# Performance work log

Hardware: AMD Instinct MI355X
Metric: run time of the kernel (lower is better)

Reference implementation:

```python
import jax, jax.numpy as jnp
import numpy as np

H = 64  # hidden_size

def _gru_layer(x_seq, Wih, Whh, bih, bhh):
    """PyTorch-semantics GRU layer. x_seq: [B, T, D] -> [B, T, H].
    Gate order in weights is (r, z, n), matching nn.GRU."""
    B = x_seq.shape[0]
    # Precompute input projections for all timesteps at once: [B, T, 3H]
    x_proj = jnp.einsum('btd,gd->btg', x_seq, Wih) + bih
    x_proj = jnp.swapaxes(x_proj, 0, 1)  # [T, B, 3H] for scan

    def step(h, xp):
        hp = h @ Whh.T + bhh                      # [B, 3H]
        xr, xz, xn = jnp.split(xp, 3, axis=-1)
        hr, hz, hn = jnp.split(hp, 3, axis=-1)
        r = jax.nn.sigmoid(xr + hr)
        z = jax.nn.sigmoid(xz + hz)
        n = jnp.tanh(xn + r * hn)
        h_new = (1.0 - z) * n + z * h
        return h_new, h_new

    h0 = jnp.zeros((B, H), dtype=x_seq.dtype)
    _, hs = jax.lax.scan(step, h0, x_proj)        # hs: [T, B, H]
    return jnp.swapaxes(hs, 0, 1)                 # [B, T, H]


def setup_inputs() -> dict:
    key = jax.random.key(0)
    ks = jax.random.split(key, 12)
    B, T, D, O = 2048, 512, 1, 1
    s = 1.0 / np.sqrt(H)  # PyTorch GRU init scale
    return {
        'x':     jax.random.normal(ks[0], (B, T, D), jnp.float32),
        'W_ih0': jax.random.normal(ks[1], (3 * H, D), jnp.float32) * s,
        'W_hh0': jax.random.normal(ks[2], (3 * H, H), jnp.float32) * s,
        'b_ih0': jax.random.normal(ks[3], (3 * H,), jnp.float32) * s,
        'b_hh0': jax.random.normal(ks[4], (3 * H,), jnp.float32) * s,
        'W_ih1': jax.random.normal(ks[5], (3 * H, H), jnp.float32) * s,
        'W_hh1': jax.random.normal(ks[6], (3 * H, H), jnp.float32) * s,
        'b_ih1': jax.random.normal(ks[7], (3 * H,), jnp.float32) * s,
        'b_hh1': jax.random.normal(ks[8], (3 * H,), jnp.float32) * s,
        'W_fc':  jax.random.normal(ks[9], (O, H), jnp.float32) * s,
        'b_fc':  jax.random.normal(ks[10], (O,), jnp.float32) * s,
    }


def reference(x, W_ih0, W_hh0, b_ih0, b_hh0, W_ih1, W_hh1, b_ih1, b_hh1, W_fc, b_fc):
    h1 = _gru_layer(x, W_ih0, W_hh0, b_ih0, b_hh0)   # [B, T, H]
    h2 = _gru_layer(h1, W_ih1, W_hh1, b_ih1, b_hh1)  # [B, T, H]
    last = h2[:, -1, :]                              # [B, H]
    return last @ W_fc.T + b_fc                      # [B, O]
```

## Files before the change

### kernel.cpp

```cpp
#include <hip/hip_runtime.h>


#define T_LEN 512
#define BROWS 16
#define XPAD  513
#define LOG2E 1.44269504088896f

typedef float          f32x4 __attribute__((ext_vector_type(4)));
typedef __bf16         bf16x8 __attribute__((ext_vector_type(8)));
typedef unsigned short us8   __attribute__((ext_vector_type(8)));
typedef unsigned int   ui4   __attribute__((ext_vector_type(4)));
typedef unsigned int   ui2   __attribute__((ext_vector_type(2)));
typedef unsigned short ushort_t;

__device__ __forceinline__ float bf2f(ushort_t b){
    unsigned int u = ((unsigned int)b) << 16;
    return __uint_as_float(u);
}
__device__ __forceinline__ ushort_t f2bf(float f){
    unsigned int u = __float_as_uint(f);
    u = (u + 0x7FFFu + ((u >> 16) & 1u)) >> 16;
    return (ushort_t)u;
}
__device__ __forceinline__ float ld_any(const void* p, int i, bool f32){
    return f32 ? ((const float*)p)[i] : bf2f(((const ushort_t*)p)[i]);
}
__device__ __forceinline__ float exp2_fast(float x){
#if __has_builtin(__builtin_amdgcn_exp2f)
    return __builtin_amdgcn_exp2f(x);
#else
    return __expf(0.6931471805599453f * x);
#endif
}
__device__ __forceinline__ float rcp_fast(float x){
#if __has_builtin(__builtin_amdgcn_rcpf)
    return __builtin_amdgcn_rcpf(x);
#else
    return __fdividef(1.0f, x);
#endif
}
__device__ __forceinline__ float sigm2(float t){
    return rcp_fast(1.0f + exp2_fast(-t));
}
__device__ __forceinline__ float tanh2(float t){
    return fmaf(-2.0f, rcp_fast(exp2_fast(t) + 1.0f), 1.0f);
}
__device__ __forceinline__ f32x4 mfma16(bf16x8 a, bf16x8 b, f32x4 c){
    return __builtin_amdgcn_mfma_f32_16x16x32_bf16(a, b, c, 0, 0, 0);
}
__device__ __forceinline__ unsigned int cvtpk(float lo, float hi){
    unsigned int r;
    asm("v_cvt_pk_bf16_f32 %0, %1, %2" : "=v"(r) : "v"(lo), "v"(hi));
    return r;
}
__device__ __forceinline__ bf16x8 mk_frag(const void* W, int n, int kb, bool f32, float sc){
    us8 tmp;
    #pragma unroll
    for (int j = 0; j < 8; ++j){
        float v = f32 ? ((const float*)W)[n * 64 + kb + j]
                      : bf2f(((const ushort_t*)W)[n * 64 + kb + j]);
        tmp[j] = f2bf(v * sc);
    }
    return __builtin_bit_cast(bf16x8, tmp);
}

__global__ __launch_bounds__(512, 2) void gru_fused(
    const void* __restrict__ xv,
    const void* __restrict__ Wih0, const void* __restrict__ Whh0,
    const void* __restrict__ bih0, const void* __restrict__ bhh0,
    const void* __restrict__ Wih1, const void* __restrict__ Whh1,
    const void* __restrict__ bih1, const void* __restrict__ bhh1,
    const void* __restrict__ Wfc,  const void* __restrict__ bfc,
    void* __restrict__ outv)
{
    __shared__ float xbuf[BROWS * XPAD];
    __shared__ ui2   hAq[2][4][64];
    __shared__ ui2   hBq[2][4][64];
    __shared__ float fcb[4][16];

    const int tid   = threadIdx.x;
    const int wv    = tid >> 6;
    const int layer = wv >> 2;
    const int tau   = wv & 3;
    const int l  = tid & 63;
    const int b  = l & 15;
    const int hp = l >> 4;
    const int am = l & 15;
    const long row0 = (long)blockIdx.x * BROWS;

    bool f32 = false;
    {
        const ushort_t* xs = (const ushort_t*)xv;
        for (int j = 0; j < 64; ++j){
            int e = (xs[2 * j] >> 7) & 0xFF;
            if (e > 150) f32 = true;
        }
    }

    {
        ui2 z = {0u, 0u};
        ui2* pa = &hAq[0][0][0];
        ui2* pb = &hBq[0][0][0];
        for (int k = tid; k < 2 * 4 * 64; k += 512){ pa[k] = z; pb[k] = z; }
    }
    if (f32){
        for (int idx = tid; idx < BROWS * (T_LEN / 4); idx += 512){
            const int r = idx >> 7, sg = idx & 127;
            f32x4 v = ((const f32x4*)((const float*)xv + (row0 + r) * T_LEN))[sg];
            #pragma unroll
            for (int j = 0; j < 4; ++j) xbuf[r * XPAD + sg * 4 + j] = v[j];
        }
    } else {
        for (int idx = tid; idx < BROWS * (T_LEN / 8); idx += 512){
            const int r = idx >> 6, sg = idx & 63;
            us8 v = ((const us8*)((const ushort_t*)xv + (row0 + r) * T_LEN))[sg];
            #pragma unroll
            for (int j = 0; j < 8; ++j) xbuf[r * XPAD + sg * 8 + j] = bf2f(v[j]);
        }
    }

    const float gsc0 = LOG2E, gsc2 = 2.0f * LOG2E;

    bf16x8 wA[3][2];
    bf16x8 wH[3][2];
    f32x4 cbR, cbZ, cbNx, cbNh;
    f32x4 cwR, cwZ, cwN;
    const void* Wihp = layer ? Wih1 : Wih0;
    const void* Whhp = layer ? Whh1 : Whh0;
    const void* bihp = layer ? bih1 : bih0;
    const void* bhhp = layer ? bhh1 : bhh0;
    const int hb0 = 32 * (tau >> 1) + 8 * hp + 4 * (tau & 1);
    #pragma unroll
    for (int g = 0; g < 3; ++g){
        const float sc = (g == 2) ? gsc2 : gsc0;
        const int grow = g * 64 + 32 * (tau >> 1) + 8 * (am >> 2) + 4 * (tau & 1) + (am & 3);
        if (layer == 0){
            wA[g][0] = mk_frag(Whhp, grow, 8 * hp,      f32, sc);
            wA[g][1] = mk_frag(Whhp, grow, 32 + 8 * hp, f32, sc);
        } else {
            wA[g][0] = mk_frag(Wihp, grow, 8 * hp,      f32, sc);
            wA[g][1] = mk_frag(Wihp, grow, 32 + 8 * hp, f32, sc);
            wH[g][0] = mk_frag(Whhp, grow, 8 * hp,      f32, sc);
            wH[g][1] = mk_frag(Whhp, grow, 32 + 8 * hp, f32, sc);
        }
    }
    #pragma unroll
    for (int r = 0; r < 4; ++r){
        const int hc = hb0 + r;
        cbR[r]  = (ld_any(bihp, hc, f32)      + ld_any(bhhp, hc, f32))      * gsc0;
        cbZ[r]  = (ld_any(bihp, 64 + hc, f32) + ld_any(bhhp, 64 + hc, f32)) * gsc0;
        cbNx[r] = ld_any(bihp, 128 + hc, f32) * gsc2;
        cbNh[r] = ld_any(bhhp, 128 + hc, f32) * gsc2;
        if (layer == 0){
            cwR[r] = ld_any(Wih0, hc, f32)       * gsc0;
            cwZ[r] = ld_any(Wih0, 64 + hc, f32)  * gsc0;
            cwN[r] = ld_any(Wih0, 128 + hc, f32) * gsc2;
        }
    }

    f32x4 hS = {0.f, 0.f, 0.f, 0.f};

    __syncthreads();

    for (int t = 0; t < T_LEN; ++t){
        if (layer == 0){
            const int p = t & 1, pr = p ^ 1;
            ui2 q0 = hAq[pr][0][l], q1 = hAq[pr][1][l];
            ui2 q2 = hAq[pr][2][l], q3 = hAq[pr][3][l];
            ui4 u0 = {q0[0], q0[1], q1[0], q1[1]};
            ui4 u1 = {q2[0], q2[1], q3[0], q3[1]};
            bf16x8 B0 = __builtin_bit_cast(bf16x8, u0);
            bf16x8 B1 = __builtin_bit_cast(bf16x8, u1);
            const float xb = xbuf[b * XPAD + t];
            f32x4 aR, aZ, aX, aN;
            #pragma unroll
            for (int r = 0; r < 4; ++r){
                aR[r] = fmaf(xb, cwR[r], cbR[r]);
                aZ[r] = fmaf(xb, cwZ[r], cbZ[r]);
                aX[r] = fmaf(xb, cwN[r], cbNx[r]);
            }
            aR = mfma16(wA[0][0], B0, aR); aR = mfma16(wA[0][1], B1, aR);
            aZ = mfma16(wA[1][0], B0, aZ); aZ = mfma16(wA[1][1], B1, aZ);
            aN = mfma16(wA[2][0], B0, cbNh); aN = mfma16(wA[2][1], B1, aN);
            #pragma unroll
            for (int r = 0; r < 4; ++r){
                float rg = sigm2(aR[r]);
                float zg = sigm2(aZ[r]);
                float ng = tanh2(aX[r] + rg * aN[r]);
                hS[r] = ng + zg * (hS[r] - ng);
            }
            ui2 own = { cvtpk(hS[0], hS[1]), cvtpk(hS[2], hS[3]) };
            hAq[p][tau][l] = own;
        } else if (t > 0){
            const int pa = (t - 1) & 1, pb = pa ^ 1;
            ui2 a0 = hAq[pa][0][l], a1 = hAq[pa][1][l];
            ui2 a2 = hAq[pa][2][l], a3 = hAq[pa][3][l];
            ui2 c0 = hBq[pb][0][l], c1 = hBq[pb][1][l];
            ui2 c2 = hBq[pb][2][l], c3 = hBq[pb][3][l];
            ui4 ua0 = {a0[0], a0[1], a1[0], a1[1]};
            ui4 ua1 = {a2[0], a2[1], a3[0], a3[1]};
            ui4 ub0 = {c0[0], c0[1], c1[0], c1[1]};
            ui4 ub1 = {c2[0], c2[1], c3[0], c3[1]};
            bf16x8 gA0 = __builtin_bit_cast(bf16x8, ua0);
            bf16x8 gA1 = __builtin_bit_cast(bf16x8, ua1);
            bf16x8 B0  = __builtin_bit_cast(bf16x8, ub0);
            bf16x8 B1  = __builtin_bit_cast(bf16x8, ub1);
            f32x4 aR, aZ, aX, aN;
            aR = mfma16(wA[0][0], gA0, cbR);  aR = mfma16(wA[0][1], gA1, aR);
            aR = mfma16(wH[0][0], B0,  aR);   aR = mfma16(wH[0][1], B1,  aR);
            aZ = mfma16(wA[1][0], gA0, cbZ);  aZ = mfma16(wA[1][1], gA1, aZ);
            aZ = mfma16(wH[1][0], B0,  aZ);   aZ = mfma16(wH[1][1], B1,  aZ);
            aX = mfma16(wA[2][0], gA0, cbNx); aX = mfma16(wA[2][1], gA1, aX);
            aN = mfma16(wH[2][0], B0,  cbNh); aN = mfma16(wH[2][1], B1,  aN);
            #pragma unroll
            for (int r = 0; r < 4; ++r){
                float rg = sigm2(aR[r]);
                float zg = sigm2(aZ[r]);
                float ng = tanh2(aX[r] + rg * aN[r]);
                hS[r] = ng + zg * (hS[r] - ng);
            }
            ui2 own = { cvtpk(hS[0], hS[1]), cvtpk(hS[2], hS[3]) };
            hBq[pa][tau][l] = own;
        }
        __syncthreads();
    }

    if (layer == 1){
        ui2 a0 = hAq[1][0][l], a1 = hAq[1][1][l];
        ui2 a2 = hAq[1][2][l], a3 = hAq[1][3][l];
        ui2 c0 = hBq[0][0][l], c1 = hBq[0][1][l];
        ui2 c2 = hBq[0][2][l], c3 = hBq[0][3][l];
        ui4 ua0 = {a0[0], a0[1], a1[0], a1[1]};
        ui4 ua1 = {a2[0], a2[1], a3[0], a3[1]};
        ui4 ub0 = {c0[0], c0[1], c1[0], c1[1]};
        ui4 ub1 = {c2[0], c2[1], c3[0], c3[1]};
        bf16x8 gA0 = __builtin_bit_cast(bf16x8, ua0);
        bf16x8 gA1 = __builtin_bit_cast(bf16x8, ua1);
        bf16x8 B0  = __builtin_bit_cast(bf16x8, ub0);
        bf16x8 B1  = __builtin_bit_cast(bf16x8, ub1);
        f32x4 aR, aZ, aX, aN;
        aR = mfma16(wA[0][0], gA0, cbR);  aR = mfma16(wA[0][1], gA1, aR);
        aR = mfma16(wH[0][0], B0,  aR);   aR = mfma16(wH[0][1], B1,  aR);
        aZ = mfma16(wA[1][0], gA0, cbZ);  aZ = mfma16(wA[1][1], gA1, aZ);
        aZ = mfma16(wH[1][0], B0,  aZ);   aZ = mfma16(wH[1][1], B1,  aZ);
        aX = mfma16(wA[2][0], gA0, cbNx); aX = mfma16(wA[2][1], gA1, aX);
        aN = mfma16(wH[2][0], B0,  cbNh); aN = mfma16(wH[2][1], B1,  aN);
        float part = 0.0f;
        #pragma unroll
        for (int r = 0; r < 4; ++r){
            float rg = sigm2(aR[r]);
            float zg = sigm2(aZ[r]);
            float ng = tanh2(aX[r] + rg * aN[r]);
            float hf = ng + zg * (hS[r] - ng);
            part = fmaf(ld_any(Wfc, hb0 + r, f32), hf, part);
        }
        part += __shfl_xor(part, 16);
        part += __shfl_xor(part, 32);
        if (l < 16) fcb[tau][b] = part;
    }
    __syncthreads();

    if (wv == 0 && l < 16){
        float s = fcb[0][b] + fcb[1][b] + fcb[2][b] + fcb[3][b]
                + ld_any(bfc, 0, f32);
        if (f32) ((float*)outv)[row0 + b] = s;
        else     ((ushort_t*)outv)[row0 + b] = f2bf(s);
    }
}

extern "C" void kernel_launch(void* const* d_in, const int* in_sizes, int n_in,
                              void* d_out, int out_size, void* d_ws, size_t ws_size,
                              hipStream_t stream)
{
    (void)in_sizes; (void)n_in; (void)d_ws; (void)ws_size;
    const int B = out_size;
    const int nblk = B / BROWS;
    gru_fused<<<nblk, 512, 0, stream>>>(
        d_in[0],
        d_in[1], d_in[2], d_in[3], d_in[4],
        d_in[5], d_in[6], d_in[7], d_in[8],
        d_in[9], d_in[10],
        d_out);
}
```

Measured before the change: 348.1 us.

## Replace per-timestep block barrier with LDS sequence-flag point-to-point sync

Replaces the __syncthreads at every timestep with per-wave sequence counters in shared memory. Each wave spins until the layer-0 and layer-1 waves it depends on have posted the needed step. Layer 1 now runs its own loop offset by one step, with the final-step FC reduction folded into that loop. The aim is to remove full-block barrier stalls so the two layers can drift relative to each other. The cost is spin-polling on LDS with s_sleep. The ordering is also fragile: the double-buffered hAq and hBq can only be overwritten safely if the waits strictly limit how far one layer gets ahead of the other.

```diff
diff --git a/kernel.cpp b/kernel.cpp
--- a/kernel.cpp
+++ b/kernel.cpp
@@ -62,6 +62,22 @@
         tmp[j] = f2bf(v * sc);
     }
     return __builtin_bit_cast(bf16x8, tmp);
+}
+__device__ __forceinline__ void wait_flags(volatile int* sa, int na,
+                                           volatile int* sb, int nb){
+    for (;;){
+        int a0 = sa[0], a1 = sa[1], a2 = sa[2], a3 = sa[3];
+        int b0 = sb[0], b1 = sb[1], b2 = sb[2], b3 = sb[3];
+        int ma = min(min(a0, a1), min(a2, a3));
+        int mb = min(min(b0, b1), min(b2, b3));
+        if (ma >= na && mb >= nb) break;
+        __builtin_amdgcn_s_sleep(1);
+    }
+    asm volatile("" ::: "memory");
+}
+__device__ __forceinline__ void post_flag(volatile int* slot, int v, int lane){
+    asm volatile("s_waitcnt lgkmcnt(0)" ::: "memory");
+    if (lane == 0) *slot = v;
 }
 
 __global__ __launch_bounds__(512, 2) void gru_fused(
@@ -77,6 +93,7 @@
     __shared__ ui2   hAq[2][4][64];
     __shared__ ui2   hBq[2][4][64];
     __shared__ float fcb[4][16];
+    __shared__ int   flags[8];
 
     const int tid   = threadIdx.x;
     const int wv    = tid >> 6;
@@ -88,6 +105,9 @@
     const int am = l & 15;
     const long row0 = (long)blockIdx.x * BROWS;
 
+    volatile int* seqA = (volatile int*)&flags[0];
+    volatile int* seqB = (volatile int*)&flags[4];
+
     bool f32 = false;
     {
         const ushort_t* xs = (const ushort_t*)xv;
@@ -102,6 +122,7 @@
         ui2* pa = &hAq[0][0][0];
         ui2* pb = &hBq[0][0][0];
         for (int k = tid; k < 2 * 4 * 64; k += 512){ pa[k] = z; pb[k] = z; }
+        if (tid < 8) flags[tid] = 0;
     }
     if (f32){
         for (int idx = tid; idx < BROWS * (T_LEN / 4); idx += 512){
@@ -162,8 +183,9 @@
 
     __syncthreads();
 
-    for (int t = 0; t < T_LEN; ++t){
-        if (layer == 0){
+    if (layer == 0){
+        for (int t = 0; t < T_LEN; ++t){
+            wait_flags(seqA, t, seqB, t - 1);
             const int p = t & 1, pr = p ^ 1;
             ui2 q0 = hAq[pr][0][l], q1 = hAq[pr][1][l];
             ui2 q2 = hAq[pr][2][l], q3 = hAq[pr][3][l];
@@ -191,7 +213,11 @@
             }
             ui2 own = { cvtpk(hS[0], hS[1]), cvtpk(hS[2], hS[3]) };
             hAq[p][tau][l] = own;
-        } else if (t > 0){
+            post_flag(&seqA[tau], t + 1, l);
+        }
+    } else {
+        for (int t = 1; t <= T_LEN; ++t){
+            wait_flags(seqA, t, seqB, t - 1);
             const int pa = (t - 1) & 1, pb = pa ^ 1;
             ui2 a0 = hAq[pa][0][l], a1 = hAq[pa][1][l];
             ui2 a2 = hAq[pa][2][l], a3 = hAq[pa][3][l];
@@ -212,52 +238,34 @@
             aZ = mfma16(wH[1][0], B0,  aZ);   aZ = mfma16(wH[1][1], B1,  aZ);
             aX = mfma16(wA[2][0], gA0, cbNx); aX = mfma16(wA[2][1], gA1, aX);
             aN = mfma16(wH[2][0], B0,  cbNh); aN = mfma16(wH[2][1], B1,  aN);
-            #pragma unroll
-            for (int r = 0; r < 4; ++r){
-                float rg = sigm2(aR[r]);
-                float zg = sigm2(aZ[r]);
-                float ng = tanh2(aX[r] + rg * aN[r]);
-                hS[r] = ng + zg * (hS[r] - ng);
+            if (t < T_LEN){
+                #pragma unroll
+                for (int r = 0; r < 4; ++r){
+                    float rg = sigm2(aR[r]);
+                    float zg = sigm2(aZ[r]);
+                    float ng = tanh2(aX[r] + rg * aN[r]);
+                    hS[r] = ng + zg * (hS[r] - ng);
+                }
+                ui2 own = { cvtpk(hS[0], hS[1]), cvtpk(hS[2], hS[3]) };
+                hBq[pa][tau][l] = own;
+                post_flag(&seqB[tau], t, l);
+            } else {
+                float part = 0.0f;
+                #pragma unroll
+                for (int r = 0; r < 4; ++r){
+                    float rg = sigm2(aR[r]);
+                    float zg = sigm2(aZ[r]);
+                    float ng = tanh2(aX[r] + rg * aN[r]);
+                    float hf = ng + zg * (hS[r] - ng);
+                    part = fmaf(ld_any(Wfc, hb0 + r, f32), hf, part);
+                }
+                part += __shfl_xor(part, 16);
+                part += __shfl_xor(part, 32);
+                if (l < 16) fcb[tau][b] = part;
             }
-            ui2 own = { cvtpk(hS[0], hS[1]), cvtpk(hS[2], hS[3]) };
-            hBq[pa][tau][l] = own;
-        }
-        __syncthreads();
-    }
-
-    if (layer == 1){
-        ui2 a0 = hAq[1][0][l], a1 = hAq[1][1][l];
-        ui2 a2 = hAq[1][2][l], a3 = hAq[1][3][l];
-        ui2 c0 = hBq[0][0][l], c1 = hBq[0][1][l];
-        ui2 c2 = hBq[0][2][l], c3 = hBq[0][3][l];
-        ui4 ua0 = {a0[0], a0[1], a1[0], a1[1]};
-        ui4 ua1 = {a2[0], a2[1], a3[0], a3[1]};
-        ui4 ub0 = {c0[0], c0[1], c1[0], c1[1]};
-        ui4 ub1 = {c2[0], c2[1], c3[0], c3[1]};
-        bf16x8 gA0 = __builtin_bit_cast(bf16x8, ua0);
-        bf16x8 gA1 = __builtin_bit_cast(bf16x8, ua1);
-        bf16x8 B0  = __builtin_bit_cast(bf16x8, ub0);
-        bf16x8 B1  = __builtin_bit_cast(bf16x8, ub1);
-        f32x4 aR, aZ, aX, aN;
-        aR = mfma16(wA[0][0], gA0, cbR);  aR = mfma16(wA[0][1], gA1, aR);
-        aR = mfma16(wH[0][0], B0,  aR);   aR = mfma16(wH[0][1], B1,  aR);
-        aZ = mfma16(wA[1][0], gA0, cbZ);  aZ = mfma16(wA[1][1], gA1, aZ);
-        aZ = mfma16(wH[1][0], B0,  aZ);   aZ = mfma16(wH[1][1], B1,  aZ);
-        aX = mfma16(wA[2][0], gA0, cbNx); aX = mfma16(wA[2][1], gA1, aX);
-        aN = mfma16(wH[2][0], B0,  cbNh); aN = mfma16(wH[2][1], B1,  aN);
-        float part = 0.0f;
-        #pragma unroll
-        for (int r = 0; r < 4; ++r){
-            float rg = sigm2(aR[r]);
-            float zg = sigm2(aZ[r]);
-            float ng = tanh2(aX[r] + rg * aN[r]);
-            float hf = ng + zg * (hS[r] - ng);
-            part = fmaf(ld_any(Wfc, hb0 + r, f32), hf, part);
-        }
-        part += __shfl_xor(part, 16);
-        part += __shfl_xor(part, 32);
-        if (l < 16) fcb[tau][b] = part;
-    }
+        }
+    }
+
     __syncthreads();
 
     if (wv == 0 && l < 16){
```

Measured after the change: 464.5 us. 1.33x slower.

## Process two 16-row batch groups per block and stream x from global

Applied to the files above, without the earlier changes.

Each block now handles 32 batch rows as two independent 16-row MFMA groups, so every timestep carries twice the work for each barrier and halves the grid to 64 blocks. The LDS staging buffer for x is removed and layer-0 waves prefetch the next timestep's input straight from global memory. This amortizes the per-step __syncthreads latency over two independent recurrences, giving the MFMA and transcendental chains room to interleave. In exchange, 64 blocks may leave many of the 256 CUs idle, and the per-step global loads add latency to the serial loop.

```diff
diff --git a/kernel.cpp b/kernel.cpp
--- a/kernel.cpp
+++ b/kernel.cpp
@@ -2,8 +2,7 @@
 
 
 #define T_LEN 512
-#define BROWS 16
-#define XPAD  513
+#define BROWS 32
 #define LOG2E 1.44269504088896f
 
 typedef float          f32x4 __attribute__((ext_vector_type(4)));
@@ -73,10 +72,9 @@
     const void* __restrict__ Wfc,  const void* __restrict__ bfc,
     void* __restrict__ outv)
 {
-    __shared__ float xbuf[BROWS * XPAD];
-    __shared__ ui2   hAq[2][4][64];
-    __shared__ ui2   hBq[2][4][64];
-    __shared__ float fcb[4][16];
+    __shared__ ui2   hAq[2][2][4][64];
+    __shared__ ui2   hBq[2][2][4][64];
+    __shared__ float fcb[2][4][16];
 
     const int tid   = threadIdx.x;
     const int wv    = tid >> 6;
@@ -99,24 +97,9 @@
 
     {
         ui2 z = {0u, 0u};
-        ui2* pa = &hAq[0][0][0];
-        ui2* pb = &hBq[0][0][0];
-        for (int k = tid; k < 2 * 4 * 64; k += 512){ pa[k] = z; pb[k] = z; }
-    }
-    if (f32){
-        for (int idx = tid; idx < BROWS * (T_LEN / 4); idx += 512){
-            const int r = idx >> 7, sg = idx & 127;
-            f32x4 v = ((const f32x4*)((const float*)xv + (row0 + r) * T_LEN))[sg];
-            #pragma unroll
-            for (int j = 0; j < 4; ++j) xbuf[r * XPAD + sg * 4 + j] = v[j];
-        }
-    } else {
-        for (int idx = tid; idx < BROWS * (T_LEN / 8); idx += 512){
-            const int r = idx >> 6, sg = idx & 63;
-            us8 v = ((const us8*)((const ushort_t*)xv + (row0 + r) * T_LEN))[sg];
-            #pragma unroll
-            for (int j = 0; j < 8; ++j) xbuf[r * XPAD + sg * 8 + j] = bf2f(v[j]);
-        }
+        ui2* pa = &hAq[0][0][0][0];
+        ui2* pb = &hBq[0][0][0][0];
+        for (int k = tid; k < 2 * 2 * 4 * 64; k += 512){ pa[k] = z; pb[k] = z; }
     }
 
     const float gsc0 = LOG2E, gsc2 = 2.0f * LOG2E;
@@ -158,49 +141,116 @@
         }
     }
 
-    f32x4 hS = {0.f, 0.f, 0.f, 0.f};
+    f32x4 hS[2] = {{0,0,0,0},{0,0,0,0}};
 
     __syncthreads();
 
-    for (int t = 0; t < T_LEN; ++t){
-        if (layer == 0){
+    if (layer == 0){
+        float xc0 = ld_any(xv, (int)((row0 + b)      * T_LEN), f32);
+        float xc1 = ld_any(xv, (int)((row0 + 16 + b) * T_LEN), f32);
+        for (int t = 0; t < T_LEN; ++t){
+            const int tn = (t + 1 < T_LEN) ? t + 1 : T_LEN - 1;
+            float xn0 = ld_any(xv, (int)((row0 + b)      * T_LEN + tn), f32);
+            float xn1 = ld_any(xv, (int)((row0 + 16 + b) * T_LEN + tn), f32);
             const int p = t & 1, pr = p ^ 1;
-            ui2 q0 = hAq[pr][0][l], q1 = hAq[pr][1][l];
-            ui2 q2 = hAq[pr][2][l], q3 = hAq[pr][3][l];
-            ui4 u0 = {q0[0], q0[1], q1[0], q1[1]};
-            ui4 u1 = {q2[0], q2[1], q3[0], q3[1]};
-            bf16x8 B0 = __builtin_bit_cast(bf16x8, u0);
-            bf16x8 B1 = __builtin_bit_cast(bf16x8, u1);
-            const float xb = xbuf[b * XPAD + t];
-            f32x4 aR, aZ, aX, aN;
+            ui2 q[2][4];
             #pragma unroll
-            for (int r = 0; r < 4; ++r){
-                aR[r] = fmaf(xb, cwR[r], cbR[r]);
-                aZ[r] = fmaf(xb, cwZ[r], cbZ[r]);
-                aX[r] = fmaf(xb, cwN[r], cbNx[r]);
-            }
-            aR = mfma16(wA[0][0], B0, aR); aR = mfma16(wA[0][1], B1, aR);
-            aZ = mfma16(wA[1][0], B0, aZ); aZ = mfma16(wA[1][1], B1, aZ);
-            aN = mfma16(wA[2][0], B0, cbNh); aN = mfma16(wA[2][1], B1, aN);
+            for (int g = 0; g < 2; ++g){
+                #pragma unroll
+                for (int k = 0; k < 4; ++k) q[g][k] = hAq[pr][g][k][l];
+            }
+            const float xcv[2] = { xc0, xc1 };
             #pragma unroll
-            for (int r = 0; r < 4; ++r){
-                float rg = sigm2(aR[r]);
-                float zg = sigm2(aZ[r]);
-                float ng = tanh2(aX[r] + rg * aN[r]);
-                hS[r] = ng + zg * (hS[r] - ng);
-            }
-            ui2 own = { cvtpk(hS[0], hS[1]), cvtpk(hS[2], hS[3]) };
-            hAq[p][tau][l] = own;
-        } else if (t > 0){
-            const int pa = (t - 1) & 1, pb = pa ^ 1;
-            ui2 a0 = hAq[pa][0][l], a1 = hAq[pa][1][l];
-            ui2 a2 = hAq[pa][2][l], a3 = hAq[pa][3][l];
-            ui2 c0 = hBq[pb][0][l], c1 = hBq[pb][1][l];
-            ui2 c2 = hBq[pb][2][l], c3 = hBq[pb][3][l];
-            ui4 ua0 = {a0[0], a0[1], a1[0], a1[1]};
-            ui4 ua1 = {a2[0], a2[1], a3[0], a3[1]};
-            ui4 ub0 = {c0[0], c0[1], c1[0], c1[1]};
-            ui4 ub1 = {c2[0], c2[1], c3[0], c3[1]};
+            for (int g = 0; g < 2; ++g){
+                ui4 u0 = {q[g][0][0], q[g][0][1], q[g][1][0], q[g][1][1]};
+                ui4 u1 = {q[g][2][0], q[g][2][1], q[g][3][0], q[g][3][1]};
+                bf16x8 B0 = __builtin_bit_cast(bf16x8, u0);
+                bf16x8 B1 = __builtin_bit_cast(bf16x8, u1);
+                const float xb = xcv[g];
+                f32x4 aR, aZ, aX, aN;
+                #pragma unroll
+                for (int r = 0; r < 4; ++r){
+                    aR[r] = fmaf(xb, cwR[r], cbR[r]);
+                    aZ[r] = fmaf(xb, cwZ[r], cbZ[r]);
+                    aX[r] = fmaf(xb, cwN[r], cbNx[r]);
+                }
+                aR = mfma16(wA[0][0], B0, aR); aR = mfma16(wA[0][1], B1, aR);
+                aZ = mfma16(wA[1][0], B0, aZ); aZ = mfma16(wA[1][1], B1, aZ);
+                aN = mfma16(wA[2][0], B0, cbNh); aN = mfma16(wA[2][1], B1, aN);
+                #pragma unroll
+                for (int r = 0; r < 4; ++r){
+                    float rg = sigm2(aR[r]);
+                    float zg = sigm2(aZ[r]);
+                    float ng = tanh2(aX[r] + rg * aN[r]);
+                    hS[g][r] = ng + zg * (hS[g][r] - ng);
+                }
+                ui2 own = { cvtpk(hS[g][0], hS[g][1]), cvtpk(hS[g][2], hS[g][3]) };
+                hAq[p][g][tau][l] = own;
+            }
+            xc0 = xn0; xc1 = xn1;
+            __syncthreads();
+        }
+    } else {
+        for (int t = 0; t < T_LEN; ++t){
+            if (t > 0){
+                const int pa = (t - 1) & 1, pb = pa ^ 1;
+                ui2 a[2][4], c[2][4];
+                #pragma unroll
+                for (int g = 0; g < 2; ++g){
+                    #pragma unroll
+                    for (int k = 0; k < 4; ++k){
+                        a[g][k] = hAq[pa][g][k][l];
+                        c[g][k] = hBq[pb][g][k][l];
+                    }
+                }
+                #pragma unroll
+                for (int g = 0; g < 2; ++g){
+                    ui4 ua0 = {a[g][0][0], a[g][0][1], a[g][1][0], a[g][1][1]};
+                    ui4 ua1 = {a[g][2][0], a[g][2][1], a[g][3][0], a[g][3][1]};
+                    ui4 ub0 = {c[g][0][0], c[g][0][1], c[g][1][0], c[g][1][1]};
+                    ui4 ub1 = {c[g][2][0], c[g][2][1], c[g][3][0], c[g][3][1]};
+                    bf16x8 gA0 = __builtin_bit_cast(bf16x8, ua0);
+                    bf16x8 gA1 = __builtin_bit_cast(bf16x8, ua1);
+                    bf16x8 B0  = __builtin_bit_cast(bf16x8, ub0);
+                    bf16x8 B1  = __builtin_bit_cast(bf16x8, ub1);
+                    f32x4 aR, aZ, aX, aN;
+                    aR = mfma16(wA[0][0], gA0, cbR);  aR = mfma16(wA[0][1], gA1, aR);
+                    aR = mfma16(wH[0][0], B0,  aR);   aR = mfma16(wH[0][1], B1,  aR);
+                    aZ = mfma16(wA[1][0], gA0, cbZ);  aZ = mfma16(wA[1][1], gA1, aZ);
+                    aZ = mfma16(wH[1][0], B0,  aZ);   aZ = mfma16(wH[1][1], B1,  aZ);
+                    aX = mfma16(wA[2][0], gA0, cbNx); aX = mfma16(wA[2][1], gA1, aX);
+                    aN = mfma16(wH[2][0], B0,  cbNh); aN = mfma16(wH[2][1], B1,  aN);
+                    #pragma unroll
+                    for (int r = 0; r < 4; ++r){
+                        float rg = sigm2(aR[r]);
+                        float zg = sigm2(aZ[r]);
+                        float ng = tanh2(aX[r] + rg * aN[r]);
+                        hS[g][r] = ng + zg * (hS[g][r] - ng);
+                    }
+                    ui2 own = { cvtpk(hS[g][0], hS[g][1]), cvtpk(hS[g][2], hS[g][3]) };
+                    hBq[pa][g][tau][l] = own;
+                }
+            }
+            __syncthreads();
+        }
+    }
+
+    if (layer == 1){
+        ui2 a[2][4], c[2][4];
+        #pragma unroll
+        for (int g = 0; g < 2; ++g){
+            #pragma unroll
+            for (int k = 0; k < 4; ++k){
+                a[g][k] = hAq[1][g][k][l];
+                c[g][k] = hBq[0][g][k][l];
+            }
+        }
+        #pragma unroll
+        for (int g = 0; g < 2; ++g){
+            ui4 ua0 = {a[g][0][0], a[g][0][1], a[g][1][0], a[g][1][1]};
+            ui4 ua1 = {a[g][2][0], a[g][2][1], a[g][3][0], a[g][3][1]};
+            ui4 ub0 = {c[g][0][0], c[g][0][1], c[g][1][0], c[g][1][1]};
+            ui4 ub1 = {c[g][2][0], c[g][2][1], c[g][3][0], c[g][3][1]};
             bf16x8 gA0 = __builtin_bit_cast(bf16x8, ua0);
             bf16x8 gA1 = __builtin_bit_cast(bf16x8, ua1);
             bf16x8 B0  = __builtin_bit_cast(bf16x8, ub0);
@@ -212,59 +262,29 @@
             aZ = mfma16(wH[1][0], B0,  aZ);   aZ = mfma16(wH[1][1], B1,  aZ);
             aX = mfma16(wA[2][0], gA0, cbNx); aX = mfma16(wA[2][1], gA1, aX);
             aN = mfma16(wH[2][0], B0,  cbNh); aN = mfma16(wH[2][1], B1,  aN);
+            float part = 0.0f;
             #pragma unroll
             for (int r = 0; r < 4; ++r){
                 float rg = sigm2(aR[r]);
                 float zg = sigm2(aZ[r]);
                 float ng = tanh2(aX[r] + rg * aN[r]);
-                hS[r] = ng + zg * (hS[r] - ng);
-            }
-            ui2 own = { cvtpk(hS[0], hS[1]), cvtpk(hS[2], hS[3]) };
-            hBq[pa][tau][l] = own;
-        }
-        __syncthreads();
-    }
-
-    if (layer == 1){
-        ui2 a0 = hAq[1][0][l], a1 = hAq[1][1][l];
-        ui2 a2 = hAq[1][2][l], a3 = hAq[1][3][l];
-        ui2 c0 = hBq[0][0][l], c1 = hBq[0][1][l];
-        ui2 c2 = hBq[0][2][l], c3 = hBq[0][3][l];
-        ui4 ua0 = {a0[0], a0[1], a1[0], a1[1]};
-        ui4 ua1 = {a2[0], a2[1], a3[0], a3[1]};
-        ui4 ub0 = {c0[0], c0[1], c1[0], c1[1]};
-        ui4 ub1 = {c2[0], c2[1], c3[0], c3[1]};
-        bf16x8 gA0 = __builtin_bit_cast(bf16x8, ua0);
-        bf16x8 gA1 = __builtin_bit_cast(bf16x8, ua1);
-        bf16x8 B0  = __builtin_bit_cast(bf16x8, ub0);
-        bf16x8 B1  = __builtin_bit_cast(bf16x8, ub1);
-        f32x4 aR, aZ, aX, aN;
-        aR = mfma16(wA[0][0], gA0, cbR);  aR = mfma16(wA[0][1], gA1, aR);
-        aR = mfma16(wH[0][0], B0,  aR);   aR = mfma16(wH[0][1], B1,  aR);
-        aZ = mfma16(wA[1][0], gA0, cbZ);  aZ = mfma16(wA[1][1], gA1, aZ);
-        aZ = mfma16(wH[1][0], B0,  aZ);   aZ = mfma16(wH[1][1], B1,  aZ);
-        aX = mfma16(wA[2][0], gA0, cbNx); aX = mfma16(wA[2][1], gA1, aX);
-        aN = mfma16(wH[2][0], B0,  cbNh); aN = mfma16(wH[2][1], B1,  aN);
-        float part = 0.0f;
-        #pragma unroll
-        for (int r = 0; r < 4; ++r){
-            float rg = sigm2(aR[r]);
-            float zg = sigm2(aZ[r]);
-            float ng = tanh2(aX[r] + rg * aN[r]);
-            float hf = ng + zg * (hS[r] - ng);
-            part = fmaf(ld_any(Wfc, hb0 + r, f32), hf, part);
-        }
-        part += __shfl_xor(part, 16);
-        part += __shfl_xor(part, 32);
-        if (l < 16) fcb[tau][b] = part;
-    }
+                float hf = ng + zg * (hS[g][r] - ng);
+                part = fmaf(ld_any(Wfc, hb0 + r, f32), hf, part);
+            }
+            part += __shfl_xor(part, 16);
+            part += __shfl_xor(part, 32);
+            if (l < 16) fcb[g][tau][b] = part;
+        }
+    }
+
     __syncthreads();
 
-    if (wv == 0 && l < 16){
-        float s = fcb[0][b] + fcb[1][b] + fcb[2][b] + fcb[3][b]
+    if (tid < 2 * 16){
+        const int g = tid >> 4, bb = tid & 15;
+        float s = fcb[g][0][bb] + fcb[g][1][bb] + fcb[g][2][bb] + fcb[g][3][bb]
                 + ld_any(bfc, 0, f32);
-        if (f32) ((float*)outv)[row0 + b] = s;
-        else     ((ushort_t*)outv)[row0 + b] = f2bf(s);
+        if (f32) ((float*)outv)[row0 + g * 16 + bb] = s;
+        else     ((ushort_t*)outv)[row0 + g * 16 + bb] = f2bf(s);
     }
 }
 
```

Result: slower. 553.4 us (+59.0%).

## Pack two independent batch groups into one 1024-thread block

Applied to the files above, without the earlier changes.

Each block now processes two 16-row batch groups with 512 threads apiece, and shared buffers gain a per-group dimension. The grid halves and launch bounds change to 1024 threads with one block. This may amortise per-block overhead, but it couples both groups to one block-wide barrier every timestep and uses fewer blocks across the CUs.

```diff
diff --git a/kernel.cpp b/kernel.cpp
--- a/kernel.cpp
+++ b/kernel.cpp
@@ -2,7 +2,7 @@
 
 
 #define T_LEN 512
-#define BROWS 16
+#define GPB   2
 #define XPAD  513
 #define LOG2E 1.44269504088896f
 
@@ -64,7 +64,7 @@
     return __builtin_bit_cast(bf16x8, tmp);
 }
 
-__global__ __launch_bounds__(512, 2) void gru_fused(
+__global__ __launch_bounds__(1024, 1) void gru_fused(
     const void* __restrict__ xv,
     const void* __restrict__ Wih0, const void* __restrict__ Whh0,
     const void* __restrict__ bih0, const void* __restrict__ bhh0,
@@ -73,20 +73,22 @@
     const void* __restrict__ Wfc,  const void* __restrict__ bfc,
     void* __restrict__ outv)
 {
-    __shared__ float xbuf[BROWS * XPAD];
-    __shared__ ui2   hAq[2][4][64];
-    __shared__ ui2   hBq[2][4][64];
-    __shared__ float fcb[4][16];
+    __shared__ float xbuf[GPB][16 * XPAD];
+    __shared__ ui2   hAq[GPB][2][4][64];
+    __shared__ ui2   hBq[GPB][2][4][64];
+    __shared__ float fcb[GPB][4][16];
 
     const int tid   = threadIdx.x;
-    const int wv    = tid >> 6;
+    const int grp   = tid >> 9;
+    const int stid  = tid & 511;
+    const int wv    = stid >> 6;
     const int layer = wv >> 2;
     const int tau   = wv & 3;
     const int l  = tid & 63;
     const int b  = l & 15;
     const int hp = l >> 4;
     const int am = l & 15;
-    const long row0 = (long)blockIdx.x * BROWS;
+    const long row0 = (long)blockIdx.x * (16 * GPB) + grp * 16;
 
     bool f32 = false;
     {
@@ -99,23 +101,23 @@
 
     {
         ui2 z = {0u, 0u};
-        ui2* pa = &hAq[0][0][0];
-        ui2* pb = &hBq[0][0][0];
-        for (int k = tid; k < 2 * 4 * 64; k += 512){ pa[k] = z; pb[k] = z; }
+        ui2* pa = &hAq[0][0][0][0];
+        ui2* pb = &hBq[0][0][0][0];
+        for (int k = tid; k < GPB * 2 * 4 * 64; k += 1024){ pa[k] = z; pb[k] = z; }
     }
     if (f32){
-        for (int idx = tid; idx < BROWS * (T_LEN / 4); idx += 512){
+        for (int idx = stid; idx < 16 * (T_LEN / 4); idx += 512){
             const int r = idx >> 7, sg = idx & 127;
             f32x4 v = ((const f32x4*)((const float*)xv + (row0 + r) * T_LEN))[sg];
             #pragma unroll
-            for (int j = 0; j < 4; ++j) xbuf[r * XPAD + sg * 4 + j] = v[j];
+            for (int j = 0; j < 4; ++j) xbuf[grp][r * XPAD + sg * 4 + j] = v[j];
         }
     } else {
-        for (int idx = tid; idx < BROWS * (T_LEN / 8); idx += 512){
+        for (int idx = stid; idx < 16 * (T_LEN / 8); idx += 512){
             const int r = idx >> 6, sg = idx & 63;
             us8 v = ((const us8*)((const ushort_t*)xv + (row0 + r) * T_LEN))[sg];
             #pragma unroll
-            for (int j = 0; j < 8; ++j) xbuf[r * XPAD + sg * 8 + j] = bf2f(v[j]);
+            for (int j = 0; j < 8; ++j) xbuf[grp][r * XPAD + sg * 8 + j] = bf2f(v[j]);
         }
     }
 
@@ -165,13 +167,13 @@
     for (int t = 0; t < T_LEN; ++t){
         if (layer == 0){
             const int p = t & 1, pr = p ^ 1;
-            ui2 q0 = hAq[pr][0][l], q1 = hAq[pr][1][l];
-            ui2 q2 = hAq[pr][2][l], q3 = hAq[pr][3][l];
+            ui2 q0 = hAq[grp][pr][0][l], q1 = hAq[grp][pr][1][l];
+            ui2 q2 = hAq[grp][pr][2][l], q3 = hAq[grp][pr][3][l];
             ui4 u0 = {q0[0], q0[1], q1[0], q1[1]};
             ui4 u1 = {q2[0], q2[1], q3[0], q3[1]};
             bf16x8 B0 = __builtin_bit_cast(bf16x8, u0);
             bf16x8 B1 = __builtin_bit_cast(bf16x8, u1);
-            const float xb = xbuf[b * XPAD + t];
+            const float xb = xbuf[grp][b * XPAD + t];
             f32x4 aR, aZ, aX, aN;
             #pragma unroll
             for (int r = 0; r < 4; ++r){
@@ -190,13 +192,13 @@
                 hS[r] = ng + zg * (hS[r] - ng);
             }
             ui2 own = { cvtpk(hS[0], hS[1]), cvtpk(hS[2], hS[3]) };
-            hAq[p][tau][l] = own;
+            hAq[grp][p][tau][l] = own;
         } else if (t > 0){
             const int pa = (t - 1) & 1, pb = pa ^ 1;
-            ui2 a0 = hAq[pa][0][l], a1 = hAq[pa][1][l];
-            ui2 a2 = hAq[pa][2][l], a3 = hAq[pa][3][l];
-            ui2 c0 = hBq[pb][0][l], c1 = hBq[pb][1][l];
-            ui2 c2 = hBq[pb][2][l], c3 = hBq[pb][3][l];
+            ui2 a0 = hAq[grp][pa][0][l], a1 = hAq[grp][pa][1][l];
+            ui2 a2 = hAq[grp][pa][2][l], a3 = hAq[grp][pa][3][l];
+            ui2 c0 = hBq[grp][pb][0][l], c1 = hBq[grp][pb][1][l];
+            ui2 c2 = hBq[grp][pb][2][l], c3 = hBq[grp][pb][3][l];
             ui4 ua0 = {a0[0], a0[1], a1[0], a1[1]};
             ui4 ua1 = {a2[0], a2[1], a3[0], a3[1]};
             ui4 ub0 = {c0[0], c0[1], c1[0], c1[1]};
@@ -220,16 +222,16 @@
                 hS[r] = ng + zg * (hS[r] - ng);
             }
             ui2 own = { cvtpk(hS[0], hS[1]), cvtpk(hS[2], hS[3]) };
-            hBq[pa][tau][l] = own;
+            hBq[grp][pa][tau][l] = own;
         }
         __syncthreads();
     }
 
     if (layer == 1){
-        ui2 a0 = hAq[1][0][l], a1 = hAq[1][1][l];
-        ui2 a2 = hAq[1][2][l], a3 = hAq[1][3][l];
-        ui2 c0 = hBq[0][0][l], c1 = hBq[0][1][l];
-        ui2 c2 = hBq[0][2][l], c3 = hBq[0][3][l];
+        ui2 a0 = hAq[grp][1][0][l], a1 = hAq[grp][1][1][l];
+        ui2 a2 = hAq[grp][1][2][l], a3 = hAq[grp][1][3][l];
+        ui2 c0 = hBq[grp][0][0][l], c1 = hBq[grp][0][1][l];
+        ui2 c2 = hBq[grp][0][2][l], c3 = hBq[grp][0][3][l];
         ui4 ua0 = {a0[0], a0[1], a1[0], a1[1]};
         ui4 ua1 = {a2[0], a2[1], a3[0], a3[1]};
         ui4 ub0 = {c0[0], c0[1], c1[0], c1[1]};
@@ -256,12 +258,12 @@
         }
         part += __shfl_xor(part, 16);
         part += __shfl_xor(part, 32);
-        if (l < 16) fcb[tau][b] = part;
+        if (l < 16) fcb[grp][tau][b] = part;
     }
     __syncthreads();
 
     if (wv == 0 && l < 16){
-        float s = fcb[0][b] + fcb[1][b] + fcb[2][b] + fcb[3][b]
+        float s = fcb[grp][0][b] + fcb[grp][1][b] + fcb[grp][2][b] + fcb[grp][3][b]
                 + ld_any(bfc, 0, f32);
         if (f32) ((float*)outv)[row0 + b] = s;
         else     ((ushort_t*)outv)[row0 + b] = f2bf(s);
@@ -274,8 +276,8 @@
 {
     (void)in_sizes; (void)n_in; (void)d_ws; (void)ws_size;
     const int B = out_size;
-    const int nblk = B / BROWS;
-    gru_fused<<<nblk, 512, 0, stream>>>(
+    const int nblk = B / (16 * GPB);
+    gru_fused<<<nblk, 1024, 0, stream>>>(
         d_in[0],
         d_in[1], d_in[2], d_in[3], d_in[4],
         d_in[5], d_in[6], d_in[7], d_in[8],
```

Result: slower. 552.4 us (+58.7%).
